# Optimization experiments

Hardware: AMD Instinct MI355X
Metric: run time of the kernel (lower is better)

## Reference

```python
import jax, jax.numpy as jnp
import numpy as np

N_AGENTS = 32
STATE_DIM = 512
EMBED = 64
BATCH = 32768


def setup_inputs() -> dict:
    key = jax.random.key(0)
    ks = jax.random.split(key, 16)
    g = lambda k, shape, fan_in: jax.random.normal(k, shape, jnp.float32) / np.sqrt(fan_in)
    return {
        "agent_qs": jax.random.normal(ks[0], (BATCH, N_AGENTS), jnp.float32),
        "states": jax.random.normal(ks[1], (BATCH, STATE_DIM), jnp.float32),
        # hyper_w1: Linear(state,E) -> ReLU -> Linear(E, n_agents*E)
        "w1_l1_w": g(ks[2], (EMBED, STATE_DIM), STATE_DIM),
        "w1_l1_b": jnp.zeros((EMBED,), jnp.float32),
        "w1_l2_w": g(ks[3], (N_AGENTS * EMBED, EMBED), EMBED),
        "w1_l2_b": jnp.zeros((N_AGENTS * EMBED,), jnp.float32),
        # hyper_w2: Linear(state,E) -> ReLU -> Linear(E, E)
        "w2_l1_w": g(ks[4], (EMBED, STATE_DIM), STATE_DIM),
        "w2_l1_b": jnp.zeros((EMBED,), jnp.float32),
        "w2_l2_w": g(ks[5], (EMBED, EMBED), EMBED),
        "w2_l2_b": jnp.zeros((EMBED,), jnp.float32),
        # hyper_b1: Linear(state, E)
        "b1_w": g(ks[6], (EMBED, STATE_DIM), STATE_DIM),
        "b1_b": jnp.zeros((EMBED,), jnp.float32),
        # hyper_b2: Linear(state,E) -> ReLU -> Linear(E, 1)
        "b2_l1_w": g(ks[7], (EMBED, STATE_DIM), STATE_DIM),
        "b2_l1_b": jnp.zeros((EMBED,), jnp.float32),
        "b2_l2_w": g(ks[8], (1, EMBED), EMBED),
        "b2_l2_b": jnp.zeros((1,), jnp.float32),
    }


def _linear(x, w, b):
    return x @ w.T + b


def reference(agent_qs, states,
              w1_l1_w, w1_l1_b, w1_l2_w, w1_l2_b,
              w2_l1_w, w2_l1_b, w2_l2_w, w2_l2_b,
              b1_w, b1_b, b2_l1_w, b2_l1_b, b2_l2_w, b2_l2_b):
    B = agent_qs.shape[0]
    # hypernetworks producing per-sample weights
    w1 = jnp.abs(_linear(jax.nn.relu(_linear(states, w1_l1_w, w1_l1_b)), w1_l2_w, w1_l2_b))
    w1 = w1.reshape(B, N_AGENTS, EMBED)                      # [B, A, E]
    b1 = _linear(states, b1_w, b1_b)                         # [B, E]
    hidden = jax.nn.elu(jnp.einsum('ba,bae->be', agent_qs, w1) + b1)  # [B, E]
    w2 = jnp.abs(_linear(jax.nn.relu(_linear(states, w2_l1_w, w2_l1_b)), w2_l2_w, w2_l2_b))  # [B, E]
    b2 = _linear(jax.nn.relu(_linear(states, b2_l1_w, b2_l1_b)), b2_l2_w, b2_l2_b)           # [B, 1]
    q_total = jnp.einsum('be,be->b', hidden, w2) + b2[:, 0]  # [B]
    return q_total
```

## Files before the change

kernel.cpp:

```cpp
#include <hip/hip_runtime.h>

typedef unsigned short u16;
typedef unsigned int u32;
typedef short bf16x8 __attribute__((ext_vector_type(8)));
typedef float f32x4 __attribute__((ext_vector_type(4)));
typedef u16 u16x4 __attribute__((ext_vector_type(4)));

#define NAG 32
#define STATE 512
#define EMBED 64
#define TB 64

#define OFF_W1L1 0
#define OFF_W2L1 32768
#define OFF_B1W  65536
#define OFF_B2L1 98304
#define OFF_W1L2 131072
#define OFF_W2L2 262144
#define WS_TOTAL 266240

__device__ __forceinline__ float bf2f(u16 u) {
    u32 i = ((u32)u) << 16; float f;
    __builtin_memcpy(&f, &i, 4); return f;
}
__device__ __forceinline__ u16 f2bf(float f) {
    u32 i; __builtin_memcpy(&i, &f, 4);
    return (u16)((i + 0x8000u) >> 16);
}
__device__ __forceinline__ bf16x8 ld8(const u16* p) {
    return *reinterpret_cast<const bf16x8*>(p);
}
__device__ __forceinline__ bf16x8 cvt8(f32x4 a, f32x4 b) {
    bf16x8 r;
#pragma unroll
    for (int i = 0; i < 4; ++i) r[i]     = (short)f2bf(a[i]);
#pragma unroll
    for (int i = 0; i < 4; ++i) r[i + 4] = (short)f2bf(b[i]);
    return r;
}
__device__ __forceinline__ void dma16(const void* g, void* l) {
    __builtin_amdgcn_global_load_lds(
        (const __attribute__((address_space(1))) u32*)g,
        (__attribute__((address_space(3))) u32*)l, 16, 0, 0);
}

#define VMW(n) __builtin_amdgcn_s_waitcnt(0x0F70 | (n))
#define BARRIER() asm volatile("s_barrier" ::: "memory")

#define STAGE_A(ksl, buf) do {                                          \
    const u16* _s = wsb + (size_t)(wave * 64 + lane) * STATE + (ksl) * 32; \
    u16* _d = &wa[buf][(wave * 64 + lane) * 8];                         \
    dma16(_s,      _d);                                                 \
    dma16(_s + 8,  _d + 2048);                                          \
    dma16(_s + 16, _d + 4096);                                          \
    dma16(_s + 24, _d + 6144);                                          \
} while (0)

#define STAGE_B(bs, buf) do {                                           \
    _Pragma("unroll")                                                   \
    for (int _j = 0; _j < 4; ++_j) {                                    \
        const int _idx = wave * 4 + _j;                                 \
        const int _c = _idx >> 1, _h = _idx & 1;                        \
        const int _r = _h * 64 + lane;                                  \
        dma16(wsb + OFF_W1L2 + ((size_t)(bs) * 128 + _r) * EMBED + _c * 8, \
              &wa[buf][(_c * 128 + _r) * 8]);                           \
    }                                                                   \
} while (0)

__global__ __launch_bounds__(256) void cvt_weights(
    const float* __restrict__ w1l1w, const float* __restrict__ w2l1w,
    const float* __restrict__ b1w,   const float* __restrict__ b2l1w,
    const float* __restrict__ w1l2w, const float* __restrict__ w2l2w,
    u16* __restrict__ ws)
{
    int idx = blockIdx.x * 256 + threadIdx.x;
    const float* src; int off;
    if      (idx < OFF_W2L1)  { src = w1l1w; off = OFF_W1L1; }
    else if (idx < OFF_B1W)   { src = w2l1w; off = OFF_W2L1; }
    else if (idx < OFF_B2L1)  { src = b1w;   off = OFF_B1W;  }
    else if (idx < OFF_W1L2)  { src = b2l1w; off = OFF_B2L1; }
    else if (idx < OFF_W2L2)  { src = w1l2w; off = OFF_W1L2; }
    else if (idx < WS_TOTAL)  { src = w2l2w; off = OFF_W2L2; }
    else return;
    ws[idx] = f2bf(src[idx - off]);
}

__global__ __launch_bounds__(256, 2) void qmix_kernel(
    const float* __restrict__ qs,    const float* __restrict__ st,
    const u16*  __restrict__ wsb,
    const float* __restrict__ w1l1b, const float* __restrict__ w1l2b,
    const float* __restrict__ w2l1b, const float* __restrict__ w2l2b,
    const float* __restrict__ b1b,   const float* __restrict__ b2l1b,
    const float* __restrict__ b2l2w, const float* __restrict__ b2l2b,
    float* __restrict__ out)
{
    __shared__ u16  wa[2][8192];
    __shared__ u16  y[TB][264];
    __shared__ u16  qsT[NAG][72];
    __shared__ u16  w1bs[2048];
    __shared__ float qacc[TB];
    __shared__ float b2wv[64];

    const int t    = threadIdx.x;
    const int wave = t >> 6, lane = t & 63;
    const int m = lane & 15, quad = lane >> 4;
    const int sbase = blockIdx.x * TB;
    const int s0 = wave * 16;

    if (t < 64) b2wv[t] = b2l2w[t];
    {
        f32x4 w0 = *reinterpret_cast<const f32x4*>(w1l2b + t * 8);
        f32x4 w1 = *reinterpret_cast<const f32x4*>(w1l2b + t * 8 + 4);
        *reinterpret_cast<bf16x8*>(&w1bs[t * 8]) = cvt8(w0, w1);
    }
    {
        const int a = t & 31, sg = (t >> 5) * 8;
#pragma unroll
        for (int k = 0; k < 8; ++k)
            qsT[a][sg + k] = f2bf(qs[(size_t)(sbase + sg + k) * NAG + a]);
    }
    float abias[16];
#pragma unroll
    for (int tt = 0; tt < 4; ++tt) abias[tt]      = w1l1b[tt * 16 + m];
#pragma unroll
    for (int tt = 0; tt < 4; ++tt) abias[tt + 4]  = w2l1b[tt * 16 + m];
#pragma unroll
    for (int tt = 0; tt < 4; ++tt) abias[tt + 8]  = b1b[tt * 16 + m];
#pragma unroll
    for (int tt = 0; tt < 4; ++tt) abias[tt + 12] = b2l1b[tt * 16 + m];

    const float* sp0 = st + (size_t)(sbase + s0 + m) * STATE + quad * 8;
    f32x4 sa0 = *reinterpret_cast<const f32x4*>(sp0);
    f32x4 sb0 = *reinterpret_cast<const f32x4*>(sp0 + 4);
    STAGE_A(0, 0);

    f32x4 acc[16] = {};
    f32x4 sa1, sb1;
    for (int s = 0; s < 16; ++s) {
        BARRIER();
        if (s < 15) {
            STAGE_A(s + 1, (s + 1) & 1);
            sa1 = *reinterpret_cast<const f32x4*>(sp0 + (s + 1) * 32);
            sb1 = *reinterpret_cast<const f32x4*>(sp0 + (s + 1) * 32 + 4);
            VMW(6);
        } else {
            STAGE_B(0, 0);
            VMW(4);
        }
        BARRIER();
        bf16x8 af = cvt8(sa0, sb0);
        const u16* wb = wa[s & 1];
#pragma unroll
        for (int tt = 0; tt < 16; ++tt) {
            const int row = tt * 16 + m;
            bf16x8 b = ld8(&wb[(quad * 256 + row) * 8]);
            acc[tt] = __builtin_amdgcn_mfma_f32_16x16x32_bf16(af, b, acc[tt], 0, 0, 0);
        }
        sa0 = sa1; sb0 = sb1;
    }
#pragma unroll
    for (int tt = 0; tt < 16; ++tt) {
        const bool isrelu = (tt < 8) || (tt >= 12);
        const int fcol = tt * 16 + m;
#pragma unroll
        for (int r = 0; r < 4; ++r) {
            float v = acc[tt][r] + abias[tt];
            if (isrelu) v = fmaxf(v, 0.f);
            y[s0 + quad * 4 + r][fcol] = f2bf(v);
        }
    }
    __syncthreads();

    const int e = wave * 16 + m;
    bf16x8 haf[4][2];
#pragma unroll
    for (int g = 0; g < 4; ++g) {
        haf[g][0] = *reinterpret_cast<const bf16x8*>(&y[g * 16 + m][quad * 8]);
        haf[g][1] = *reinterpret_cast<const bf16x8*>(&y[g * 16 + m][32 + quad * 8]);
    }

    f32x4 hacc[4] = {};
    for (int bs = 0; bs < 16; ++bs) {
        BARRIER();
        if (bs < 15) {
            STAGE_B(bs + 1, (bs + 1) & 1);
            VMW(4);
        } else {
            VMW(0);
        }
        BARRIER();
        const u16* wb = wa[bs & 1];
#pragma unroll
        for (int aloc = 0; aloc < 2; ++aloc) {
            const int row = aloc * 64 + wave * 16 + m;
            bf16x8 b0 = ld8(&wb[(quad * 128 + row) * 8]);
            bf16x8 b1 = ld8(&wb[((4 + quad) * 128 + row) * 8]);
            const int a = bs * 2 + aloc;
            const float bias = bf2f(w1bs[a * EMBED + e]);
#pragma unroll
            for (int g = 0; g < 4; ++g) {
                f32x4 p = {};
                p = __builtin_amdgcn_mfma_f32_16x16x32_bf16(haf[g][0], b0, p, 0, 0, 0);
                p = __builtin_amdgcn_mfma_f32_16x16x32_bf16(haf[g][1], b1, p, 0, 0, 0);
                u16x4 qv = *reinterpret_cast<const u16x4*>(&qsT[a][g * 16 + quad * 4]);
#pragma unroll
                for (int r = 0; r < 4; ++r)
                    hacc[g][r] += bf2f((u16)qv[r]) * fabsf(p[r] + bias);
            }
        }
    }
    __syncthreads();
    u16* hid = (u16*)wa;
#pragma unroll
    for (int g = 0; g < 4; ++g)
#pragma unroll
        for (int r = 0; r < 4; ++r) {
            const int s = g * 16 + quad * 4 + r;
            float v = hacc[g][r] + bf2f(y[s][128 + e]);
            v = (v > 0.f) ? v : (__expf(v) - 1.f);
            hid[s * 66 + e] = f2bf(v);
        }
    __syncthreads();

    bf16x8 h2f0 = *reinterpret_cast<const bf16x8*>(&y[s0 + m][64 + quad * 8]);
    bf16x8 h2f1 = *reinterpret_cast<const bf16x8*>(&y[s0 + m][96 + quad * 8]);

    f32x4 qp = {};
#pragma unroll
    for (int tp = 0; tp < 4; ++tp) {
        const u16* wc = wsb + OFF_W2L2 + (size_t)(tp * 16 + m) * EMBED + quad * 8;
        bf16x8 b0 = ld8(wc);
        bf16x8 b1 = ld8(wc + 32);
        f32x4 p = {};
        p = __builtin_amdgcn_mfma_f32_16x16x32_bf16(h2f0, b0, p, 0, 0, 0);
        p = __builtin_amdgcn_mfma_f32_16x16x32_bf16(h2f1, b1, p, 0, 0, 0);
        const float bias = w2l2b[tp * 16 + m];
#pragma unroll
        for (int r = 0; r < 4; ++r)
            qp[r] += bf2f(hid[(s0 + quad * 4 + r) * 66 + tp * 16 + m]) * fabsf(p[r] + bias);
    }
#pragma unroll
    for (int off = 1; off < 16; off <<= 1) {
#pragma unroll
        for (int r = 0; r < 4; ++r) qp[r] += __shfl_xor(qp[r], off, 64);
    }
    if (m == 0) {
#pragma unroll
        for (int r = 0; r < 4; ++r) qacc[s0 + quad * 4 + r] = qp[r];
    }
    __syncthreads();

    if (t < TB) {
        float q = qacc[t] + b2l2b[0];
        float acc2 = 0.f;
#pragma unroll
        for (int kk = 0; kk < 8; ++kk) {
            bf16x8 hv = *reinterpret_cast<const bf16x8*>(&y[t][192 + kk * 8]);
#pragma unroll
            for (int j = 0; j < 8; ++j)
                acc2 += bf2f((u16)hv[j]) * b2wv[kk * 8 + j];
        }
        out[sbase + t] = q + acc2;
    }
}

extern "C" void kernel_launch(void* const* d_in, const int* in_sizes, int n_in,
                              void* d_out, int out_size, void* d_ws, size_t ws_size,
                              hipStream_t stream)
{
    const float* qs    = (const float*)d_in[0];
    const float* st    = (const float*)d_in[1];
    const float* w1l1w = (const float*)d_in[2];
    const float* w1l1b = (const float*)d_in[3];
    const float* w1l2w = (const float*)d_in[4];
    const float* w1l2b = (const float*)d_in[5];
    const float* w2l1w = (const float*)d_in[6];
    const float* w2l1b = (const float*)d_in[7];
    const float* w2l2w = (const float*)d_in[8];
    const float* w2l2b = (const float*)d_in[9];
    const float* b1w   = (const float*)d_in[10];
    const float* b1b   = (const float*)d_in[11];
    const float* b2l1w = (const float*)d_in[12];
    const float* b2l1b = (const float*)d_in[13];
    const float* b2l2w = (const float*)d_in[14];
    const float* b2l2b = (const float*)d_in[15];

    u16* wsb = (u16*)d_ws;

    cvt_weights<<<(WS_TOTAL + 255) / 256, 256, 0, stream>>>(
        w1l1w, w2l1w, b1w, b2l1w, w1l2w, w2l2w, wsb);

    int B = in_sizes[0] / NAG;
    int grid = B / TB;
    qmix_kernel<<<grid, 256, 0, stream>>>(
        qs, st, wsb,
        w1l1b, w1l2b, w2l1b, w2l2b, b1b, b2l1b, b2l2w, b2l2b,
        (float*)d_out);
}
```

Baseline: 169.9 us.

## Pre-swizzle weights into MFMA fragment order and load directly into registers

The weight conversion kernel now writes the layer-1 and w1 layer-2 weights in per-lane MFMA fragment order. The main kernel therefore loads B operands straight from global memory into double-buffered registers, replacing the LDS staging through global_load_lds and the barriers around it. This removes LDS traffic and block-wide synchronisation from both GEMM loops, and LDS use drops because the staging buffer is gone. In exchange the register footprint grows (32 prefetched bf16x8 fragments), which risks spills under the 2-blocks-per-SM launch bound, and every wave now reads the weights from L2 on its own instead of sharing them through LDS.

```diff
diff --git a/kernel.cpp b/kernel.cpp
--- a/kernel.cpp
+++ b/kernel.cpp
@@ -11,13 +11,10 @@
 #define EMBED 64
 #define TB 64
 
-#define OFF_W1L1 0
-#define OFF_W2L1 32768
-#define OFF_B1W  65536
-#define OFF_B2L1 98304
-#define OFF_W1L2 131072
-#define OFF_W2L2 262144
-#define WS_TOTAL 266240
+#define OFF_FRAGA 0
+#define OFF_FRAGB 131072
+#define OFF_W2L2  262144
+#define WS_TOTAL  266240
 
 __device__ __forceinline__ float bf2f(u16 u) {
     u32 i = ((u32)u) << 16; float f;
@@ -38,34 +35,6 @@
     for (int i = 0; i < 4; ++i) r[i + 4] = (short)f2bf(b[i]);
     return r;
 }
-__device__ __forceinline__ void dma16(const void* g, void* l) {
-    __builtin_amdgcn_global_load_lds(
-        (const __attribute__((address_space(1))) u32*)g,
-        (__attribute__((address_space(3))) u32*)l, 16, 0, 0);
-}
-
-#define VMW(n) __builtin_amdgcn_s_waitcnt(0x0F70 | (n))
-#define BARRIER() asm volatile("s_barrier" ::: "memory")
-
-#define STAGE_A(ksl, buf) do {                                          \
-    const u16* _s = wsb + (size_t)(wave * 64 + lane) * STATE + (ksl) * 32; \
-    u16* _d = &wa[buf][(wave * 64 + lane) * 8];                         \
-    dma16(_s,      _d);                                                 \
-    dma16(_s + 8,  _d + 2048);                                          \
-    dma16(_s + 16, _d + 4096);                                          \
-    dma16(_s + 24, _d + 6144);                                          \
-} while (0)
-
-#define STAGE_B(bs, buf) do {                                           \
-    _Pragma("unroll")                                                   \
-    for (int _j = 0; _j < 4; ++_j) {                                    \
-        const int _idx = wave * 4 + _j;                                 \
-        const int _c = _idx >> 1, _h = _idx & 1;                        \
-        const int _r = _h * 64 + lane;                                  \
-        dma16(wsb + OFF_W1L2 + ((size_t)(bs) * 128 + _r) * EMBED + _c * 8, \
-              &wa[buf][(_c * 128 + _r) * 8]);                           \
-    }                                                                   \
-} while (0)
 
 __global__ __launch_bounds__(256) void cvt_weights(
     const float* __restrict__ w1l1w, const float* __restrict__ w2l1w,
@@ -74,15 +43,28 @@
     u16* __restrict__ ws)
 {
     int idx = blockIdx.x * 256 + threadIdx.x;
-    const float* src; int off;
-    if      (idx < OFF_W2L1)  { src = w1l1w; off = OFF_W1L1; }
-    else if (idx < OFF_B1W)   { src = w2l1w; off = OFF_W2L1; }
-    else if (idx < OFF_B2L1)  { src = b1w;   off = OFF_B1W;  }
-    else if (idx < OFF_W1L2)  { src = b2l1w; off = OFF_B2L1; }
-    else if (idx < OFF_W2L2)  { src = w1l2w; off = OFF_W1L2; }
-    else if (idx < WS_TOTAL)  { src = w2l2w; off = OFF_W2L2; }
-    else return;
-    ws[idx] = f2bf(src[idx - off]);
+    if (idx >= WS_TOTAL) return;
+    float v;
+    if (idx < OFF_FRAGB) {
+        const int j = idx & 7, lane = (idx >> 3) & 63, tmp = idx >> 9;
+        const int tt = tmp & 15, ks = tmp >> 4;
+        const int m = lane & 15, quad = lane >> 4;
+        const int row = tt * 16 + m, col = ks * 32 + quad * 8 + j;
+        const int r = row & 63;
+        const float* src = (row < 64) ? w1l1w : (row < 128) ? w2l1w
+                          : (row < 192) ? b1w : b2l1w;
+        v = src[r * STATE + col];
+    } else if (idx < OFF_W2L2) {
+        const int local = idx - OFF_FRAGB;
+        const int j = local & 7, lane = (local >> 3) & 63, rest = local >> 9;
+        const int wv = rest & 3, h = (rest >> 2) & 1, a = rest >> 3;
+        const int m = lane & 15, quad = lane >> 4;
+        const int row = a * 64 + wv * 16 + m, col = h * 32 + quad * 8 + j;
+        v = w1l2w[row * EMBED + col];
+    } else {
+        v = w2l2w[idx - OFF_W2L2];
+    }
+    ws[idx] = f2bf(v);
 }
 
 __global__ __launch_bounds__(256, 2) void qmix_kernel(
@@ -94,8 +76,8 @@
     const float* __restrict__ b2l2w, const float* __restrict__ b2l2b,
     float* __restrict__ out)
 {
-    __shared__ u16  wa[2][8192];
     __shared__ u16  y[TB][264];
+    __shared__ u16  hidb[TB][72];
     __shared__ u16  qsT[NAG][72];
     __shared__ u16  w1bs[2048];
     __shared__ float qacc[TB];
@@ -119,6 +101,33 @@
         for (int k = 0; k < 8; ++k)
             qsT[a][sg + k] = f2bf(qs[(size_t)(sbase + sg + k) * NAG + a]);
     }
+
+    const u16* pfA = wsb + lane * 8;
+    const float* sp0 = st + (size_t)(sbase + s0 + m) * STATE + quad * 8;
+
+    bf16x8 bb[2][16];
+    f32x4 sa[2], sb[2];
+#pragma unroll
+    for (int tt = 0; tt < 16; ++tt) bb[0][tt] = ld8(pfA + tt * 512);
+    sa[0] = *reinterpret_cast<const f32x4*>(sp0);
+    sb[0] = *reinterpret_cast<const f32x4*>(sp0 + 4);
+
+    f32x4 acc[16] = {};
+#pragma unroll
+    for (int ks = 0; ks < 16; ++ks) {
+        const int cur = ks & 1, nxt = cur ^ 1;
+        if (ks < 15) {
+#pragma unroll
+            for (int tt = 0; tt < 16; ++tt)
+                bb[nxt][tt] = ld8(pfA + ((ks + 1) * 16 + tt) * 512);
+            sa[nxt] = *reinterpret_cast<const f32x4*>(sp0 + (ks + 1) * 32);
+            sb[nxt] = *reinterpret_cast<const f32x4*>(sp0 + (ks + 1) * 32 + 4);
+        }
+        bf16x8 af = cvt8(sa[cur], sb[cur]);
+#pragma unroll
+        for (int tt = 0; tt < 16; ++tt)
+            acc[tt] = __builtin_amdgcn_mfma_f32_16x16x32_bf16(af, bb[cur][tt], acc[tt], 0, 0, 0);
+    }
     float abias[16];
 #pragma unroll
     for (int tt = 0; tt < 4; ++tt) abias[tt]      = w1l1b[tt * 16 + m];
@@ -128,36 +137,6 @@
     for (int tt = 0; tt < 4; ++tt) abias[tt + 8]  = b1b[tt * 16 + m];
 #pragma unroll
     for (int tt = 0; tt < 4; ++tt) abias[tt + 12] = b2l1b[tt * 16 + m];
-
-    const float* sp0 = st + (size_t)(sbase + s0 + m) * STATE + quad * 8;
-    f32x4 sa0 = *reinterpret_cast<const f32x4*>(sp0);
-    f32x4 sb0 = *reinterpret_cast<const f32x4*>(sp0 + 4);
-    STAGE_A(0, 0);
-
-    f32x4 acc[16] = {};
-    f32x4 sa1, sb1;
-    for (int s = 0; s < 16; ++s) {
-        BARRIER();
-        if (s < 15) {
-            STAGE_A(s + 1, (s + 1) & 1);
-            sa1 = *reinterpret_cast<const f32x4*>(sp0 + (s + 1) * 32);
-            sb1 = *reinterpret_cast<const f32x4*>(sp0 + (s + 1) * 32 + 4);
-            VMW(6);
-        } else {
-            STAGE_B(0, 0);
-            VMW(4);
-        }
-        BARRIER();
-        bf16x8 af = cvt8(sa0, sb0);
-        const u16* wb = wa[s & 1];
-#pragma unroll
-        for (int tt = 0; tt < 16; ++tt) {
-            const int row = tt * 16 + m;
-            bf16x8 b = ld8(&wb[(quad * 256 + row) * 8]);
-            acc[tt] = __builtin_amdgcn_mfma_f32_16x16x32_bf16(af, b, acc[tt], 0, 0, 0);
-        }
-        sa0 = sa1; sb0 = sb1;
-    }
 #pragma unroll
     for (int tt = 0; tt < 16; ++tt) {
         const bool isrelu = (tt < 8) || (tt >= 12);
@@ -179,38 +158,41 @@
         haf[g][1] = *reinterpret_cast<const bf16x8*>(&y[g * 16 + m][32 + quad * 8]);
     }
 
+    const u16* pfB = wsb + OFF_FRAGB + (size_t)wave * 512 + lane * 8;
+    bf16x8 wb[2][2][2];
+#pragma unroll
+    for (int al = 0; al < 2; ++al)
+#pragma unroll
+        for (int h = 0; h < 2; ++h)
+            wb[0][al][h] = ld8(pfB + (al * 2 + h) * 2048);
+
     f32x4 hacc[4] = {};
-    for (int bs = 0; bs < 16; ++bs) {
-        BARRIER();
-        if (bs < 15) {
-            STAGE_B(bs + 1, (bs + 1) & 1);
-            VMW(4);
-        } else {
-            VMW(0);
-        }
-        BARRIER();
-        const u16* wb = wa[bs & 1];
-#pragma unroll
-        for (int aloc = 0; aloc < 2; ++aloc) {
-            const int row = aloc * 64 + wave * 16 + m;
-            bf16x8 b0 = ld8(&wb[(quad * 128 + row) * 8]);
-            bf16x8 b1 = ld8(&wb[((4 + quad) * 128 + row) * 8]);
-            const int a = bs * 2 + aloc;
+#pragma unroll
+    for (int p = 0; p < 16; ++p) {
+        const int cur = p & 1, nxt = cur ^ 1;
+        if (p < 15) {
+#pragma unroll
+            for (int al = 0; al < 2; ++al)
+#pragma unroll
+                for (int h = 0; h < 2; ++h)
+                    wb[nxt][al][h] = ld8(pfB + (((p + 1) * 2 + al) * 2 + h) * 2048);
+        }
+#pragma unroll
+        for (int al = 0; al < 2; ++al) {
+            const int a = p * 2 + al;
             const float bias = bf2f(w1bs[a * EMBED + e]);
 #pragma unroll
             for (int g = 0; g < 4; ++g) {
-                f32x4 p = {};
-                p = __builtin_amdgcn_mfma_f32_16x16x32_bf16(haf[g][0], b0, p, 0, 0, 0);
-                p = __builtin_amdgcn_mfma_f32_16x16x32_bf16(haf[g][1], b1, p, 0, 0, 0);
+                f32x4 pp = {};
+                pp = __builtin_amdgcn_mfma_f32_16x16x32_bf16(haf[g][0], wb[cur][al][0], pp, 0, 0, 0);
+                pp = __builtin_amdgcn_mfma_f32_16x16x32_bf16(haf[g][1], wb[cur][al][1], pp, 0, 0, 0);
                 u16x4 qv = *reinterpret_cast<const u16x4*>(&qsT[a][g * 16 + quad * 4]);
 #pragma unroll
                 for (int r = 0; r < 4; ++r)
-                    hacc[g][r] += bf2f((u16)qv[r]) * fabsf(p[r] + bias);
+                    hacc[g][r] += bf2f((u16)qv[r]) * fabsf(pp[r] + bias);
             }
         }
     }
-    __syncthreads();
-    u16* hid = (u16*)wa;
 #pragma unroll
     for (int g = 0; g < 4; ++g)
 #pragma unroll
@@ -218,7 +200,7 @@
             const int s = g * 16 + quad * 4 + r;
             float v = hacc[g][r] + bf2f(y[s][128 + e]);
             v = (v > 0.f) ? v : (__expf(v) - 1.f);
-            hid[s * 66 + e] = f2bf(v);
+            hidb[s][e] = f2bf(v);
         }
     __syncthreads();
 
@@ -237,7 +219,7 @@
         const float bias = w2l2b[tp * 16 + m];
 #pragma unroll
         for (int r = 0; r < 4; ++r)
-            qp[r] += bf2f(hid[(s0 + quad * 4 + r) * 66 + tp * 16 + m]) * fabsf(p[r] + bias);
+            qp[r] += bf2f(hidb[s0 + quad * 4 + r][tp * 16 + m]) * fabsf(p[r] + bias);
     }
 #pragma unroll
     for (int off = 1; off < 16; off <<= 1) {
```

Result: slower. 188.7 us (+11.1%).
